# Performance work log

Measured on AMD Instinct MI355X. Metric: run time of the kernel, lower is better.

The kernel has to match this reference:

```python
import jax, jax.numpy as jnp
import numpy as np

B, H, W = 8, 512, 512
K = 3            # kernel_size
PAD = (K - 1) // 2
K2 = K * K       # 9 taps


def setup_inputs() -> dict:
    key = jax.random.key(0)
    k1, k2, k3 = jax.random.split(key, 3)
    depth = jax.random.normal(k1, (B, 1, H, W), dtype=jnp.float32)
    weight = jax.random.uniform(k2, (B, K2, H, W), dtype=jnp.float32)      # per-pixel modulation mask
    offset = jax.random.normal(k3, (B, 2 * K2, H, W), dtype=jnp.float32)   # interleaved (dy, dx) per tap
    return {"depth": depth, "weight": weight, "offset": offset}


def _bilinear_gather(img, py, px):
    # img: [B, H, W]; py, px: [B, K2, H, W] sampling coords (zero outside boundaries)
    Bv, Hv, Wv = img.shape
    y0 = jnp.floor(py)
    x0 = jnp.floor(px)
    ty = py - y0
    tx = px - x0
    y0i = y0.astype(jnp.int32)
    x0i = x0.astype(jnp.int32)
    img_flat = img.reshape(Bv, -1)

    def corner(yi, xi, w):
        valid = (yi >= 0) & (yi < Hv) & (xi >= 0) & (xi < Wv)
        yc = jnp.clip(yi, 0, Hv - 1)
        xc = jnp.clip(xi, 0, Wv - 1)
        idx = (yc * Wv + xc).reshape(Bv, -1)
        vals = jnp.take_along_axis(img_flat, idx, axis=1).reshape(yi.shape)
        return jnp.where(valid, vals, 0.0) * w

    return (corner(y0i, x0i, (1.0 - ty) * (1.0 - tx))
            + corner(y0i, x0i + 1, (1.0 - ty) * tx)
            + corner(y0i + 1, x0i, ty * (1.0 - tx))
            + corner(y0i + 1, x0i + 1, ty * tx))


def reference(depth, weight, offset):
    # dkn_residual=True path: subtract per-pixel mean over the 9 taps
    w = weight - jnp.mean(weight, axis=1, keepdims=True)            # [B, 9, H, W]
    dy = offset[:, 0::2]                                             # [B, 9, H, W]
    dx = offset[:, 1::2]
    ky, kx = jnp.meshgrid(jnp.arange(K), jnp.arange(K), indexing="ij")
    ky = ky.reshape(-1).astype(jnp.float32)                          # [9]
    kx = kx.reshape(-1).astype(jnp.float32)
    gy = jnp.arange(H, dtype=jnp.float32)
    gx = jnp.arange(W, dtype=jnp.float32)
    # sampling coords: output pos - pad + tap offset + learned offset
    py = dy + gy[None, None, :, None] - PAD + ky[None, :, None, None]
    px = dx + gx[None, None, None, :] - PAD + kx[None, :, None, None]
    sampled = _bilinear_gather(depth[:, 0], py, px)                  # [B, 9, H, W]
    # dcn.weight == ones, dcn.bias == zeros -> mask-weighted sum over taps
    out = jnp.sum(sampled * w, axis=1, keepdims=True)                # [B, 1, H, W]
    return out + depth                                               # residual
```

## Files before the change

### kernel.cpp

```cpp
#include <hip/hip_runtime.h>

#define BB 8
#define HH 512
#define WW 512
#define K2 9
#define PAD 1
#define HW (HH * WW)

__global__ __launch_bounds__(256) void pp_deconv_kernel(
    const float* __restrict__ depth,
    const float* __restrict__ weight,
    const float* __restrict__ offset,
    float* __restrict__ out)
{
    int idx = blockIdx.x * blockDim.x + threadIdx.x;
    if (idx >= BB * HW) return;

    int b = idx >> 18;
    int p = idx & (HW - 1);
    int y = p >> 9;
    int x = p & (WW - 1);

    const float* wp   = weight + (size_t)b * K2 * HW + p;
    const float* op   = offset + (size_t)b * 2 * K2 * HW + p;
    const float* dimg = depth  + (size_t)b * HW;

    float wv[K2];
    float wsum = 0.f;
#pragma unroll
    for (int k = 0; k < K2; ++k) {
        wv[k] = wp[k * HW];
        wsum += wv[k];
    }
    const float wmean = wsum * (1.0f / 9.0f);

    float acc = 0.f;
#pragma unroll
    for (int k = 0; k < K2; ++k) {
        const int ky = k / 3;
        const int kx = k % 3;
        const float dy = op[(2 * k) * HW];
        const float dx = op[(2 * k + 1) * HW];

        const float py = dy + (float)(y - PAD + ky);
        const float px = dx + (float)(x - PAD + kx);

        const float y0f = floorf(py);
        const float x0f = floorf(px);
        const float ty = py - y0f;
        const float tx = px - x0f;
        const int y0 = (int)y0f;
        const int x0 = (int)x0f;
        const int y1 = y0 + 1;
        const int x1 = x0 + 1;

        const int y0c = min(max(y0, 0), HH - 1);
        const int y1c = min(max(y1, 0), HH - 1);
        const int x0c = min(max(x0, 0), WW - 1);
        const int x1c = min(max(x1, 0), WW - 1);

        const bool vy0 = (y0 >= 0) & (y0 < HH);
        const bool vy1 = (y1 >= 0) & (y1 < HH);
        const bool vx0 = (x0 >= 0) & (x0 < WW);
        const bool vx1 = (x1 >= 0) & (x1 < WW);

        const float v00 = dimg[y0c * WW + x0c];
        const float v01 = dimg[y0c * WW + x1c];
        const float v10 = dimg[y1c * WW + x0c];
        const float v11 = dimg[y1c * WW + x1c];

        const float w00 = (vy0 & vx0) ? (1.f - ty) * (1.f - tx) : 0.f;
        const float w01 = (vy0 & vx1) ? (1.f - ty) * tx         : 0.f;
        const float w10 = (vy1 & vx0) ? ty * (1.f - tx)         : 0.f;
        const float w11 = (vy1 & vx1) ? ty * tx                 : 0.f;

        const float s = v00 * w00 + v01 * w01 + v10 * w10 + v11 * w11;
        acc += s * (wv[k] - wmean);
    }

    out[idx] = acc + dimg[p];
}

extern "C" void kernel_launch(void* const* d_in, const int* in_sizes, int n_in,
                              void* d_out, int out_size, void* d_ws, size_t ws_size,
                              hipStream_t stream) {
    const float* depth  = (const float*)d_in[0];
    const float* weight = (const float*)d_in[1];
    const float* offset = (const float*)d_in[2];
    float* out = (float*)d_out;

    const int total = BB * HW;
    const int block = 256;
    const int grid = (total + block - 1) / block;
    pp_deconv_kernel<<<grid, block, 0, stream>>>(depth, weight, offset, out);
}
```

Measured before the change: 279.0 us.

## Process four pixels per thread with float4 streams and paired bilinear loads

Result: slower. 297.2 us (+6.5%).

```diff
diff --git a/kernel.cpp b/kernel.cpp
--- a/kernel.cpp
+++ b/kernel.cpp
@@ -4,81 +4,98 @@
 #define HH 512
 #define WW 512
 #define K2 9
-#define PAD 1
 #define HW (HH * WW)
 
-__global__ __launch_bounds__(256) void pp_deconv_kernel(
+struct f2 { float lo, hi; };
+
+__device__ __forceinline__ float bil(const float* __restrict__ dimg,
+                                     float py, float px) {
+    const float y0f = floorf(py);
+    const float x0f = floorf(px);
+    const float ty = py - y0f;
+    const float tx = px - x0f;
+    const int y0 = (int)y0f;
+    const int x0 = (int)x0f;
+    const int y1 = y0 + 1;
+    const int x1 = x0 + 1;
+
+    const int y0c = min(max(y0, 0), HH - 1);
+    const int y1c = min(max(y1, 0), HH - 1);
+    const int xl  = min(max(x0, 0), WW - 2);
+
+    const f2 top = *(const f2*)(dimg + y0c * WW + xl);
+    const f2 bot = *(const f2*)(dimg + y1c * WW + xl);
+
+    const bool sw = (x0 != xl);
+    const float v00 = sw ? top.hi : top.lo;
+    const float v01 = sw ? top.lo : top.hi;
+    const float v10 = sw ? bot.hi : bot.lo;
+    const float v11 = sw ? bot.lo : bot.hi;
+
+    const bool vy0 = (y0 >= 0) & (y0 < HH);
+    const bool vy1 = (y1 >= 0) & (y1 < HH);
+    const bool vx0 = (x0 >= 0) & (x0 < WW);
+    const bool vx1 = (x1 >= 0) & (x1 < WW);
+
+    const float w00 = (vy0 & vx0) ? (1.f - ty) * (1.f - tx) : 0.f;
+    const float w01 = (vy0 & vx1) ? (1.f - ty) * tx         : 0.f;
+    const float w10 = (vy1 & vx0) ? ty * (1.f - tx)         : 0.f;
+    const float w11 = (vy1 & vx1) ? ty * tx                 : 0.f;
+
+    return v00 * w00 + v01 * w01 + v10 * w10 + v11 * w11;
+}
+
+__global__ __launch_bounds__(256, 4) void pp_deconv_kernel(
     const float* __restrict__ depth,
     const float* __restrict__ weight,
     const float* __restrict__ offset,
     float* __restrict__ out)
 {
-    int idx = blockIdx.x * blockDim.x + threadIdx.x;
-    if (idx >= BB * HW) return;
-
-    int b = idx >> 18;
-    int p = idx & (HW - 1);
-    int y = p >> 9;
-    int x = p & (WW - 1);
+    const int t = blockIdx.x * blockDim.x + threadIdx.x;
+    const int idx = t << 2;
+    const int b = idx >> 18;
+    const int p = idx & (HW - 1);
+    const int y = p >> 9;
+    const int x = p & (WW - 1);
 
     const float* wp   = weight + (size_t)b * K2 * HW + p;
     const float* op   = offset + (size_t)b * 2 * K2 * HW + p;
     const float* dimg = depth  + (size_t)b * HW;
 
-    float wv[K2];
-    float wsum = 0.f;
+    float4 w4[K2];
+    float4 ws = make_float4(0.f, 0.f, 0.f, 0.f);
 #pragma unroll
     for (int k = 0; k < K2; ++k) {
-        wv[k] = wp[k * HW];
-        wsum += wv[k];
+        w4[k] = *(const float4*)(wp + k * HW);
+        ws.x += w4[k].x; ws.y += w4[k].y; ws.z += w4[k].z; ws.w += w4[k].w;
     }
-    const float wmean = wsum * (1.0f / 9.0f);
+    const float c = 1.0f / 9.0f;
+    const float4 wm = make_float4(ws.x * c, ws.y * c, ws.z * c, ws.w * c);
 
-    float acc = 0.f;
+    float4 acc = make_float4(0.f, 0.f, 0.f, 0.f);
 #pragma unroll
     for (int k = 0; k < K2; ++k) {
         const int ky = k / 3;
         const int kx = k % 3;
-        const float dy = op[(2 * k) * HW];
-        const float dx = op[(2 * k + 1) * HW];
+        const float4 dy4 = *(const float4*)(op + (2 * k) * HW);
+        const float4 dx4 = *(const float4*)(op + (2 * k + 1) * HW);
 
-        const float py = dy + (float)(y - PAD + ky);
-        const float px = dx + (float)(x - PAD + kx);
+        const float ybase = (float)(y - 1 + ky);
+        const float xbase = (float)(x - 1 + kx);
 
-        const float y0f = floorf(py);
-        const float x0f = floorf(px);
-        const float ty = py - y0f;
-        const float tx = px - x0f;
-        const int y0 = (int)y0f;
-        const int x0 = (int)x0f;
-        const int y1 = y0 + 1;
-        const int x1 = x0 + 1;
-
-        const int y0c = min(max(y0, 0), HH - 1);
-        const int y1c = min(max(y1, 0), HH - 1);
-        const int x0c = min(max(x0, 0), WW - 1);
-        const int x1c = min(max(x1, 0), WW - 1);
-
-        const bool vy0 = (y0 >= 0) & (y0 < HH);
-        const bool vy1 = (y1 >= 0) & (y1 < HH);
-        const bool vx0 = (x0 >= 0) & (x0 < WW);
-        const bool vx1 = (x1 >= 0) & (x1 < WW);
-
-        const float v00 = dimg[y0c * WW + x0c];
-        const float v01 = dimg[y0c * WW + x1c];
-        const float v10 = dimg[y1c * WW + x0c];
-        const float v11 = dimg[y1c * WW + x1c];
-
-        const float w00 = (vy0 & vx0) ? (1.f - ty) * (1.f - tx) : 0.f;
-        const float w01 = (vy0 & vx1) ? (1.f - ty) * tx         : 0.f;
-        const float w10 = (vy1 & vx0) ? ty * (1.f - tx)         : 0.f;
-        const float w11 = (vy1 & vx1) ? ty * tx                 : 0.f;
-
-        const float s = v00 * w00 + v01 * w01 + v10 * w10 + v11 * w11;
-        acc += s * (wv[k] - wmean);
+        acc.x += bil(dimg, dy4.x + ybase, dx4.x + xbase + 0.f) * (w4[k].x - wm.x);
+        acc.y += bil(dimg, dy4.y + ybase, dx4.y + xbase + 1.f) * (w4[k].y - wm.y);
+        acc.z += bil(dimg, dy4.z + ybase, dx4.z + xbase + 2.f) * (w4[k].z - wm.z);
+        acc.w += bil(dimg, dy4.w + ybase, dx4.w + xbase + 3.f) * (w4[k].w - wm.w);
     }
 
-    out[idx] = acc + dimg[p];
+    const float4 d0 = *(const float4*)(dimg + p);
+    float4 o;
+    o.x = acc.x + d0.x;
+    o.y = acc.y + d0.y;
+    o.z = acc.z + d0.z;
+    o.w = acc.w + d0.w;
+    *(float4*)(out + idx) = o;
 }
 
 extern "C" void kernel_launch(void* const* d_in, const int* in_sizes, int n_in,
@@ -89,8 +106,8 @@
     const float* offset = (const float*)d_in[2];
     float* out = (float*)d_out;
 
-    const int total = BB * HW;
+    const int total_threads = BB * HW / 4;
     const int block = 256;
-    const int grid = (total + block - 1) / block;
+    const int grid = total_threads / block;
     pp_deconv_kernel<<<grid, block, 0, stream>>>(depth, weight, offset, out);
 }
```

## Stage depth tile in LDS with halo, vectorize four pixels per thread

Applied to the files above, without the earlier changes.

Result: no change. 277.8 us (-0.4%).

```diff
diff --git a/kernel.cpp b/kernel.cpp
--- a/kernel.cpp
+++ b/kernel.cpp
@@ -4,81 +4,130 @@
 #define HH 512
 #define WW 512
 #define K2 9
-#define PAD 1
 #define HW (HH * WW)
 
-__global__ __launch_bounds__(256) void pp_deconv_kernel(
+#define TX 64
+#define TY 16
+#define NROWS (TY + 11)
+#define NCOLS (TX + 11)
+#define STRIDE (NCOLS + 1)
+
+__device__ __noinline__ float gsample(const float* __restrict__ dimg,
+                                      float py, float px) {
+    const float y0f = floorf(py);
+    const float x0f = floorf(px);
+    const float ty = py - y0f;
+    const float tx = px - x0f;
+    const int y0 = (int)y0f, x0 = (int)x0f;
+    const int y1 = y0 + 1,   x1 = x0 + 1;
+    const int y0c = min(max(y0, 0), HH - 1);
+    const int y1c = min(max(y1, 0), HH - 1);
+    const int x0c = min(max(x0, 0), WW - 1);
+    const int x1c = min(max(x1, 0), WW - 1);
+    const float v00 = dimg[y0c * WW + x0c];
+    const float v01 = dimg[y0c * WW + x1c];
+    const float v10 = dimg[y1c * WW + x0c];
+    const float v11 = dimg[y1c * WW + x1c];
+    const bool vy0 = (unsigned)y0 < HH, vy1 = (unsigned)y1 < HH;
+    const bool vx0 = (unsigned)x0 < WW, vx1 = (unsigned)x1 < WW;
+    const float w00 = (vy0 & vx0) ? (1.f - ty) * (1.f - tx) : 0.f;
+    const float w01 = (vy0 & vx1) ? (1.f - ty) * tx         : 0.f;
+    const float w10 = (vy1 & vx0) ? ty * (1.f - tx)         : 0.f;
+    const float w11 = (vy1 & vx1) ? ty * tx                 : 0.f;
+    return v00 * w00 + v01 * w01 + v10 * w10 + v11 * w11;
+}
+
+__global__ __launch_bounds__(256, 4) void pp_deconv_kernel(
     const float* __restrict__ depth,
     const float* __restrict__ weight,
     const float* __restrict__ offset,
     float* __restrict__ out)
 {
-    int idx = blockIdx.x * blockDim.x + threadIdx.x;
-    if (idx >= BB * HW) return;
+    __shared__ float tile[NROWS * STRIDE];
 
-    int b = idx >> 18;
-    int p = idx & (HW - 1);
-    int y = p >> 9;
-    int x = p & (WW - 1);
+    const int tid = threadIdx.x;
+    const int tx0 = blockIdx.x * TX;
+    const int ty0 = blockIdx.y * TY;
+    const int b   = blockIdx.z;
 
-    const float* wp   = weight + (size_t)b * K2 * HW + p;
-    const float* op   = offset + (size_t)b * 2 * K2 * HW + p;
-    const float* dimg = depth  + (size_t)b * HW;
+    const int ry0 = ty0 - 5;
+    const int cx0 = tx0 - 5;
 
-    float wv[K2];
-    float wsum = 0.f;
-#pragma unroll
-    for (int k = 0; k < K2; ++k) {
-        wv[k] = wp[k * HW];
-        wsum += wv[k];
+    const float* dimg = depth + (size_t)b * HW;
+
+    for (int li = tid; li < NROWS * NCOLS; li += 256) {
+        const int r = li / NCOLS;
+        const int c = li - r * NCOLS;
+        const int gy = ry0 + r;
+        const int gx = cx0 + c;
+        float v = 0.f;
+        if ((unsigned)gy < HH && (unsigned)gx < WW) v = dimg[gy * WW + gx];
+        tile[r * STRIDE + c] = v;
     }
-    const float wmean = wsum * (1.0f / 9.0f);
+    __syncthreads();
 
-    float acc = 0.f;
+    const int xl = (tid & 15) << 2;
+    const int yl = tid >> 4;
+    const int x = tx0 + xl;
+    const int y = ty0 + yl;
+    const int p = y * WW + x;
+
+    const float* wp = weight + (size_t)b * K2 * HW + p;
+    const float* op = offset + (size_t)b * 2 * K2 * HW + p;
+
+    float4 accw = make_float4(0.f, 0.f, 0.f, 0.f);
+    float4 accs = make_float4(0.f, 0.f, 0.f, 0.f);
+    float4 wsum = make_float4(0.f, 0.f, 0.f, 0.f);
+
 #pragma unroll
     for (int k = 0; k < K2; ++k) {
         const int ky = k / 3;
         const int kx = k % 3;
-        const float dy = op[(2 * k) * HW];
-        const float dx = op[(2 * k + 1) * HW];
+        const float4 w4  = *(const float4*)(wp + k * HW);
+        const float4 dy4 = *(const float4*)(op + (2 * k) * HW);
+        const float4 dx4 = *(const float4*)(op + (2 * k + 1) * HW);
 
-        const float py = dy + (float)(y - PAD + ky);
-        const float px = dx + (float)(x - PAD + kx);
+        const float ybase = (float)(y - 1 + ky);
+        const float xbase = (float)(x - 1 + kx);
 
-        const float y0f = floorf(py);
-        const float x0f = floorf(px);
-        const float ty = py - y0f;
-        const float tx = px - x0f;
-        const int y0 = (int)y0f;
-        const int x0 = (int)x0f;
-        const int y1 = y0 + 1;
-        const int x1 = x0 + 1;
-
-        const int y0c = min(max(y0, 0), HH - 1);
-        const int y1c = min(max(y1, 0), HH - 1);
-        const int x0c = min(max(x0, 0), WW - 1);
-        const int x1c = min(max(x1, 0), WW - 1);
-
-        const bool vy0 = (y0 >= 0) & (y0 < HH);
-        const bool vy1 = (y1 >= 0) & (y1 < HH);
-        const bool vx0 = (x0 >= 0) & (x0 < WW);
-        const bool vx1 = (x1 >= 0) & (x1 < WW);
-
-        const float v00 = dimg[y0c * WW + x0c];
-        const float v01 = dimg[y0c * WW + x1c];
-        const float v10 = dimg[y1c * WW + x0c];
-        const float v11 = dimg[y1c * WW + x1c];
-
-        const float w00 = (vy0 & vx0) ? (1.f - ty) * (1.f - tx) : 0.f;
-        const float w01 = (vy0 & vx1) ? (1.f - ty) * tx         : 0.f;
-        const float w10 = (vy1 & vx0) ? ty * (1.f - tx)         : 0.f;
-        const float w11 = (vy1 & vx1) ? ty * tx                 : 0.f;
-
-        const float s = v00 * w00 + v01 * w01 + v10 * w10 + v11 * w11;
-        acc += s * (wv[k] - wmean);
+        float s[4];
+        const float pys[4] = {dy4.x + ybase, dy4.y + ybase, dy4.z + ybase, dy4.w + ybase};
+        const float pxs[4] = {dx4.x + xbase, dx4.y + xbase + 1.f,
+                              dx4.z + xbase + 2.f, dx4.w + xbase + 3.f};
+#pragma unroll
+        for (int j = 0; j < 4; ++j) {
+            const float py = pys[j], px = pxs[j];
+            const float y0f = floorf(py);
+            const float x0f = floorf(px);
+            const float ty = py - y0f;
+            const float tx = px - x0f;
+            const int iy = (int)y0f - ry0;
+            const int ix = (int)x0f - cx0;
+            if ((unsigned)iy < NROWS - 1 && (unsigned)ix < NCOLS - 1) {
+                const float* q = tile + iy * STRIDE + ix;
+                const float v00 = q[0], v01 = q[1];
+                const float v10 = q[STRIDE], v11 = q[STRIDE + 1];
+                const float a0 = v00 + tx * (v01 - v00);
+                const float a1 = v10 + tx * (v11 - v10);
+                s[j] = a0 + ty * (a1 - a0);
+            } else {
+                s[j] = gsample(dimg, py, px);
+            }
+        }
+        accw.x += s[0] * w4.x;  accs.x += s[0];  wsum.x += w4.x;
+        accw.y += s[1] * w4.y;  accs.y += s[1];  wsum.y += w4.y;
+        accw.z += s[2] * w4.z;  accs.z += s[2];  wsum.z += w4.z;
+        accw.w += s[3] * w4.w;  accs.w += s[3];  wsum.w += w4.w;
     }
 
-    out[idx] = acc + dimg[p];
+    const float* dq = tile + (yl + 5) * STRIDE + (xl + 5);
+    const float c9 = 1.0f / 9.0f;
+    float4 o;
+    o.x = accw.x - wsum.x * c9 * accs.x + dq[0];
+    o.y = accw.y - wsum.y * c9 * accs.y + dq[1];
+    o.z = accw.z - wsum.z * c9 * accs.z + dq[2];
+    o.w = accw.w - wsum.w * c9 * accs.w + dq[3];
+    *(float4*)(out + (size_t)b * HW + p) = o;
 }
 
 extern "C" void kernel_launch(void* const* d_in, const int* in_sizes, int n_in,
@@ -89,8 +138,7 @@
     const float* offset = (const float*)d_in[2];
     float* out = (float*)d_out;
 
-    const int total = BB * HW;
-    const int block = 256;
-    const int grid = (total + block - 1) / block;
+    dim3 grid(WW / TX, HH / TY, BB);
+    dim3 block(256);
     pp_deconv_kernel<<<grid, block, 0, stream>>>(depth, weight, offset, out);
 }
```
